# Kernel tuning notes

Hardware: AMD Instinct MI355X
Metric: run time of the kernel (lower is better)

## Reference

```python
import jax, jax.numpy as jnp
import numpy as np

EPS = 1e-5

def _conv(x, w):
    # x: [B,C,H,W], w: [K,C,3,3] -> [B,K,H,W]; stacks all centroid convs into one conv
    return jax.lax.conv_general_dilated(
        x, w, window_strides=(1, 1), padding=((1, 1), (1, 1)),
        dimension_numbers=("NCHW", "OIHW", "NCHW"))

def _bn(x, gamma, beta, mean, var):
    # inference-mode BatchNorm2d over channel axis 1
    inv = gamma / jnp.sqrt(var + EPS)
    return x * inv[None, :, None, None] + (beta - mean * inv)[None, :, None, None]

def setup_inputs() -> dict:
    key = jax.random.key(0)
    ks = jax.random.split(key, 16)
    B, C, H, W, K = 32, 256, 56, 56, 16
    d = {}
    d["x"] = jax.random.normal(ks[0], (B, C, H, W), jnp.float32)
    d["w1"] = jax.random.normal(ks[1], (K, C, 3, 3), jnp.float32) * 0.05
    d["b1"] = jax.random.normal(ks[2], (K,), jnp.float32) * 0.05
    d["w2"] = jax.random.normal(ks[3], (K, C, 3, 3), jnp.float32) * 0.05
    d["b2"] = jax.random.normal(ks[4], (K,), jnp.float32) * 0.05
    d["gamma1"] = jax.random.uniform(ks[5], (C,), jnp.float32)
    d["beta1"] = jax.random.normal(ks[6], (C,), jnp.float32) * 0.1
    d["mean1"] = jax.random.normal(ks[7], (C,), jnp.float32) * 0.1
    d["var1"] = jax.random.uniform(ks[8], (C,), jnp.float32)
    d["gamma2"] = jax.random.uniform(ks[9], (C,), jnp.float32)
    d["beta2"] = jax.random.normal(ks[10], (C,), jnp.float32) * 0.1
    d["mean2"] = jax.random.normal(ks[11], (C,), jnp.float32) * 0.1
    d["var2"] = jax.random.uniform(ks[12], (C,), jnp.float32)
    d["labels1"] = jax.random.randint(ks[13], (C,), 0, K, jnp.int64)
    d["labels2"] = jax.random.randint(ks[14], (C,), 0, K, jnp.int64)
    return d

def reference(x, w1, b1, w2, b2, gamma1, beta1, mean1, var1,
              gamma2, beta2, mean2, var2, labels1, labels2):
    # centroids_apply: run all K centroid convs at once, then label-indexed
    # channel gather (equivalent to the original per-centroid conv + concat)
    y1 = _conv(x, w1)[:, labels1] + b1[labels1][None, :, None, None]
    h = jax.nn.relu(_bn(y1, gamma1, beta1, mean1, var1))
    y2 = _conv(h, w2)[:, labels2] + b2[labels2][None, :, None, None]
    out = _bn(y2, gamma2, beta2, mean2, var2) + x  # identity residual (no skipper)
    return jax.nn.relu(out)
```

## Files before the change

kernel.cpp:

```cpp
#include <hip/hip_runtime.h>
#include <cstddef>
#include <cstdint>

typedef short short8 __attribute__((ext_vector_type(8)));
typedef float f32x4 __attribute__((ext_vector_type(4)));

namespace {
constexpr int B = 32, C = 256, H = 56, W = 56, K = 16;
constexpr int HW = H * W;
constexpr int WP = 58, PP = 58 * 58;
constexpr float EPS = 1e-5f;

constexpr size_t OFF_WF1 = 0;
constexpr size_t OFF_WF2 = 73728;
constexpr size_t OFF_A1 = 147456, OFF_D1 = 148480;
constexpr size_t OFF_A2 = 149504, OFF_D2 = 150528;
constexpr size_t OFF_G1 = 151552, OFF_G2 = 152576;
constexpr size_t OFF_XT = 153600;
constexpr size_t XT_BYTES = (size_t)B * PP * C * 2;
constexpr size_t OFF_HB = OFF_XT + XT_BYTES;
constexpr int BORDER_U4 = 2 * 32 * 228 * 32;
}

__device__ inline ushort f2bf(float f) {
  uint32_t u = __float_as_uint(f);
  u += 0x7fff + ((u >> 16) & 1);
  return (ushort)(u >> 16);
}

__global__ __launch_bounds__(256) void prep_kernel(
    const float* __restrict__ w1, const float* __restrict__ b1,
    const float* __restrict__ w2, const float* __restrict__ b2,
    const float* __restrict__ gamma1, const float* __restrict__ beta1,
    const float* __restrict__ mean1, const float* __restrict__ var1,
    const float* __restrict__ gamma2, const float* __restrict__ beta2,
    const float* __restrict__ mean2, const float* __restrict__ var2,
    const int* __restrict__ lab1, const int* __restrict__ lab2,
    char* __restrict__ wsb) {
  int bid = blockIdx.x, tid = threadIdx.x;
  if (bid < 288) {
    int i = bid * 256 + tid;
    int which = i >= 36864;
    int ii = which ? i - 36864 : i;
    int j = ii & 7, lane = (ii >> 3) & 63, cc = (ii >> 9) & 7, t = ii >> 12;
    int c = cc * 32 + ((lane >> 4) << 3) + j;
    int k = lane & 15;
    const float* w = which ? w2 : w1;
    ushort* wf = (ushort*)(wsb + (which ? OFF_WF2 : OFF_WF1));
    wf[ii] = f2bf(w[k * (C * 9) + c * 9 + t]);
    if (i < C) {
      int g1 = lab1[i], g2 = lab2[i];
      float a1 = gamma1[i] / sqrtf(var1[i] + EPS);
      float a2 = gamma2[i] / sqrtf(var2[i] + EPS);
      ((float*)(wsb + OFF_A1))[i] = a1;
      ((float*)(wsb + OFF_D1))[i] = a1 * b1[g1] + beta1[i] - mean1[i] * a1;
      ((float*)(wsb + OFF_A2))[i] = a2;
      ((float*)(wsb + OFF_D2))[i] = a2 * b2[g2] + beta2[i] - mean2[i] * a2;
      ((int*)(wsb + OFF_G1))[i] = g1;
      ((int*)(wsb + OFF_G2))[i] = g2;
    }
  } else {
    int idx = (bid - 288) * 256 + tid;
    if (idx < BORDER_U4) {
      int which = idx >= (BORDER_U4 / 2);
      int j = which ? idx - BORDER_U4 / 2 : idx;
      int pix = j >> 5, q = j & 31;
      int b = pix / 228, e = pix - b * 228;
      int y, x;
      if (e < 58) { y = 0; x = e; }
      else if (e < 116) { y = 57; x = e - 58; }
      else if (e < 172) { y = e - 115; x = 0; }
      else { y = e - 171; x = 57; }
      size_t off = ((size_t)b * PP + y * WP + x) * C * 2 + (size_t)q * 16;
      int4 z = {0, 0, 0, 0};
      *(int4*)(wsb + (which ? OFF_HB : OFF_XT) + off) = z;
    }
  }
}

__global__ __launch_bounds__(256) void transpose_kernel(
    const float* __restrict__ x, char* __restrict__ wsb) {
  __shared__ float t[64][65];
  int bid = blockIdx.x;
  int b = bid / 196, rem = bid - b * 196, pt = rem >> 2, ct = rem & 3;
  int p0 = pt * 64, c0 = ct * 64;
  int tid = threadIdx.x, lane = tid & 63, grp = tid >> 6;
  const float* xb = x + ((size_t)b * C + c0) * HW + p0;
#pragma unroll
  for (int r = 0; r < 16; ++r) {
    int row = r * 4 + grp;
    t[row][lane] = xb[(size_t)row * HW + lane];
  }
  __syncthreads();
  ushort* xt = (ushort*)(wsb + OFF_XT) + (size_t)b * PP * C;
  int c2 = (tid & 31) * 2, g = tid >> 5;
#pragma unroll
  for (int r = 0; r < 8; ++r) {
    int prow = r * 8 + g;
    int p = p0 + prow;
    int y = p / 56, xx = p - y * 56;
    uint v = (uint)f2bf(t[c2][prow]) | ((uint)f2bf(t[c2 + 1][prow]) << 16);
    *(uint*)(xt + ((size_t)(y + 1) * WP + xx + 1) * C + c0 + c2) = v;
  }
}

__global__ __launch_bounds__(256) void conv1_kernel(char* __restrict__ wsb) {
  __shared__ float zs[128 * 17];
  int tid = threadIdx.x, lane = tid & 63, wave = tid >> 6;
  int row = lane & 15, blk = lane >> 4;
  int gpb = blockIdx.x * 128 + wave * 32;
  const ushort* xt = (const ushort*)(wsb + OFF_XT);
  const ushort* wfl = (const ushort*)(wsb + OFF_WF1) + lane * 8;

  int gp0 = gpb + row, gp1 = gpb + 16 + row;
  int b0 = gp0 / HW, r0 = gp0 - b0 * HW, y0 = r0 / 56, x0 = r0 - y0 * 56;
  int b1_ = gp1 / HW, r1 = gp1 - b1_ * HW, y1 = r1 / 56, x1 = r1 - y1 * 56;
  const ushort* ap0 = xt + ((size_t)b0 * PP + (y0 + 1) * WP + (x0 + 1)) * C;
  const ushort* ap1 = xt + ((size_t)b1_ * PP + (y1 + 1) * WP + (x1 + 1)) * C;

  f32x4 acc0 = {0.f, 0.f, 0.f, 0.f}, acc1 = {0.f, 0.f, 0.f, 0.f};
#pragma unroll
  for (int t = 0; t < 9; ++t) {
    const int toff = ((t / 3 - 1) * WP + (t % 3 - 1)) * C;
#pragma unroll
    for (int cc = 0; cc < 8; ++cc) {
      short8 bf = *(const short8*)(wfl + (t * 8 + cc) * 512);
      int ko = toff + cc * 32 + blk * 8;
      short8 a0 = *(const short8*)(ap0 + ko);
      short8 a1 = *(const short8*)(ap1 + ko);
      acc0 = __builtin_amdgcn_mfma_f32_16x16x32_bf16(a0, bf, acc0, 0, 0, 0);
      acc1 = __builtin_amdgcn_mfma_f32_16x16x32_bf16(a1, bf, acc1, 0, 0, 0);
    }
  }
#pragma unroll
  for (int i = 0; i < 4; ++i) {
    zs[(wave * 32 + blk * 4 + i) * 17 + row] = acc0[i];
    zs[(wave * 32 + 16 + blk * 4 + i) * 17 + row] = acc1[i];
  }
  __syncthreads();

  f32x4 a_ = *(const f32x4*)((const float*)(wsb + OFF_A1) + lane * 4);
  f32x4 d_ = *(const f32x4*)((const float*)(wsb + OFF_D1) + lane * 4);
  int4 g_ = *(const int4*)((const int*)(wsb + OFF_G1) + lane * 4);
  ushort* hb = (ushort*)(wsb + OFF_HB);
  for (int px = 0; px < 32; ++px) {
    int gp = gpb + px;
    int b = gp / HW, r = gp - b * HW, y = r / 56, xx = r - y * 56;
    const float* zr = zs + (wave * 32 + px) * 17;
    float h0 = fmaxf(fmaf(a_.x, zr[g_.x], d_.x), 0.f);
    float h1 = fmaxf(fmaf(a_.y, zr[g_.y], d_.y), 0.f);
    float h2 = fmaxf(fmaf(a_.z, zr[g_.z], d_.z), 0.f);
    float h3 = fmaxf(fmaf(a_.w, zr[g_.w], d_.w), 0.f);
    uint2 v;
    v.x = (uint)f2bf(h0) | ((uint)f2bf(h1) << 16);
    v.y = (uint)f2bf(h2) | ((uint)f2bf(h3) << 16);
    *(uint2*)(hb + ((size_t)b * PP + (y + 1) * WP + (xx + 1)) * C + lane * 4) = v;
  }
}

__global__ __launch_bounds__(256) void conv2_kernel(
    const float* __restrict__ x, char* __restrict__ wsb,
    float* __restrict__ out) {
  __shared__ float zs[128 * 17];
  int tid = threadIdx.x, lane = tid & 63, wave = tid >> 6;
  int row = lane & 15, blk = lane >> 4;
  int gpb = blockIdx.x * 128 + wave * 32;
  const ushort* hbuf = (const ushort*)(wsb + OFF_HB);
  const ushort* wfl = (const ushort*)(wsb + OFF_WF2) + lane * 8;

  int gp0 = gpb + row, gp1 = gpb + 16 + row;
  int b0 = gp0 / HW, r0 = gp0 - b0 * HW, y0 = r0 / 56, x0 = r0 - y0 * 56;
  int b1_ = gp1 / HW, r1 = gp1 - b1_ * HW, y1 = r1 / 56, x1 = r1 - y1 * 56;
  const ushort* ap0 = hbuf + ((size_t)b0 * PP + (y0 + 1) * WP + (x0 + 1)) * C;
  const ushort* ap1 = hbuf + ((size_t)b1_ * PP + (y1 + 1) * WP + (x1 + 1)) * C;

  f32x4 acc0 = {0.f, 0.f, 0.f, 0.f}, acc1 = {0.f, 0.f, 0.f, 0.f};
#pragma unroll
  for (int t = 0; t < 9; ++t) {
    const int toff = ((t / 3 - 1) * WP + (t % 3 - 1)) * C;
#pragma unroll
    for (int cc = 0; cc < 8; ++cc) {
      short8 bf = *(const short8*)(wfl + (t * 8 + cc) * 512);
      int ko = toff + cc * 32 + blk * 8;
      short8 a0 = *(const short8*)(ap0 + ko);
      short8 a1 = *(const short8*)(ap1 + ko);
      acc0 = __builtin_amdgcn_mfma_f32_16x16x32_bf16(a0, bf, acc0, 0, 0, 0);
      acc1 = __builtin_amdgcn_mfma_f32_16x16x32_bf16(a1, bf, acc1, 0, 0, 0);
    }
  }
#pragma unroll
  for (int i = 0; i < 4; ++i) {
    zs[(wave * 32 + blk * 4 + i) * 17 + row] = acc0[i];
    zs[(wave * 32 + 16 + blk * 4 + i) * 17 + row] = acc1[i];
  }
  __syncthreads();

  const float* A2p = (const float*)(wsb + OFF_A2);
  const float* D2p = (const float*)(wsb + OFF_D2);
  const int* G2p = (const int*)(wsb + OFF_G2);
  int pl = lane & 31, ch = lane >> 5;
  int gp = gpb + pl;
  int b = gp / HW, r = gp - b * HW;
  const float* zrow = zs + (wave * 32 + pl) * 17;
  const float* xp = x + (size_t)b * C * HW + r;
  float* op = out + (size_t)b * C * HW + r;
#pragma unroll 4
  for (int cl = 0; cl < 128; ++cl) {
    int c = cl * 2 + ch;
    float a = A2p[c], dd = D2p[c];
    int g = G2p[c];
    float v = fmaf(a, zrow[g], dd) + xp[(size_t)c * HW];
    op[(size_t)c * HW] = fmaxf(v, 0.f);
  }
}

extern "C" void kernel_launch(void* const* d_in, const int* in_sizes, int n_in,
                              void* d_out, int out_size, void* d_ws,
                              size_t ws_size, hipStream_t stream) {
  const float* x = (const float*)d_in[0];
  const float* w1 = (const float*)d_in[1];
  const float* b1 = (const float*)d_in[2];
  const float* w2 = (const float*)d_in[3];
  const float* b2 = (const float*)d_in[4];
  const float* gamma1 = (const float*)d_in[5];
  const float* beta1 = (const float*)d_in[6];
  const float* mean1 = (const float*)d_in[7];
  const float* var1 = (const float*)d_in[8];
  const float* gamma2 = (const float*)d_in[9];
  const float* beta2 = (const float*)d_in[10];
  const float* mean2 = (const float*)d_in[11];
  const float* var2 = (const float*)d_in[12];
  const int* lab1 = (const int*)d_in[13];
  const int* lab2 = (const int*)d_in[14];
  char* wsb = (char*)d_ws;
  float* out = (float*)d_out;

  prep_kernel<<<288 + 1824, 256, 0, stream>>>(
      w1, b1, w2, b2, gamma1, beta1, mean1, var1, gamma2, beta2, mean2, var2,
      lab1, lab2, wsb);
  transpose_kernel<<<32 * 196, 256, 0, stream>>>(x, wsb);
  conv1_kernel<<<(B * HW) / 128, 256, 0, stream>>>(wsb);
  conv2_kernel<<<(B * HW) / 128, 256, 0, stream>>>(x, wsb, out);
}
```

Before: 404.6 us.

## Stage conv inputs in swizzled LDS and store compact 16-channel conv1 outputs

Each conv block now covers two image rows of one batch image. It stages the padded input tile in double-buffered, XOR-swizzled shared memory, so the 3x3 taps reuse LDS data instead of issuing repeated global loads. Conv1 now writes only the raw 16 centroid outputs. Conv2 rebuilds the 256-channel BN+ReLU activation in shared memory from those 16 values, which removes the full bf16 intermediate buffer and its border zeroing. The residual epilogue moves into a separate vectorized kernel. The costs are an extra launch, heavy LDS use that limits occupancy, and idle MFMA slots on one wave because 112 pixels split unevenly across 4 waves.

```diff
diff --git a/kernel.cpp b/kernel.cpp
--- a/kernel.cpp
+++ b/kernel.cpp
@@ -18,8 +18,9 @@
 constexpr size_t OFF_G1 = 151552, OFF_G2 = 152576;
 constexpr size_t OFF_XT = 153600;
 constexpr size_t XT_BYTES = (size_t)B * PP * C * 2;
-constexpr size_t OFF_HB = OFF_XT + XT_BYTES;
-constexpr int BORDER_U4 = 2 * 32 * 228 * 32;
+constexpr size_t OFF_Z1 = OFF_XT + XT_BYTES;
+constexpr size_t OFF_Z2 = OFF_Z1 + (size_t)B * HW * 16 * 4;
+constexpr int BORDER_U4 = 32 * 228 * 32;
 }
 
 __device__ inline ushort f2bf(float f) {
@@ -62,18 +63,16 @@
   } else {
     int idx = (bid - 288) * 256 + tid;
     if (idx < BORDER_U4) {
-      int which = idx >= (BORDER_U4 / 2);
-      int j = which ? idx - BORDER_U4 / 2 : idx;
-      int pix = j >> 5, q = j & 31;
+      int pix = idx >> 5, q = idx & 31;
       int b = pix / 228, e = pix - b * 228;
       int y, x;
       if (e < 58) { y = 0; x = e; }
       else if (e < 116) { y = 57; x = e - 58; }
       else if (e < 172) { y = e - 115; x = 0; }
       else { y = e - 171; x = 57; }
-      size_t off = ((size_t)b * PP + y * WP + x) * C * 2 + (size_t)q * 16;
+      size_t off = OFF_XT + ((size_t)b * PP + y * WP + x) * 512 + (size_t)q * 16;
       int4 z = {0, 0, 0, 0};
-      *(int4*)(wsb + (which ? OFF_HB : OFF_XT) + off) = z;
+      *(int4*)(wsb + off) = z;
     }
   }
 }
@@ -104,113 +103,246 @@
   }
 }
 
-__global__ __launch_bounds__(256) void conv1_kernel(char* __restrict__ wsb) {
-  __shared__ float zs[128 * 17];
-  int tid = threadIdx.x, lane = tid & 63, wave = tid >> 6;
-  int row = lane & 15, blk = lane >> 4;
-  int gpb = blockIdx.x * 128 + wave * 32;
-  const ushort* xt = (const ushort*)(wsb + OFF_XT);
-  const ushort* wfl = (const ushort*)(wsb + OFF_WF1) + lane * 8;
-
-  int gp0 = gpb + row, gp1 = gpb + 16 + row;
-  int b0 = gp0 / HW, r0 = gp0 - b0 * HW, y0 = r0 / 56, x0 = r0 - y0 * 56;
-  int b1_ = gp1 / HW, r1 = gp1 - b1_ * HW, y1 = r1 / 56, x1 = r1 - y1 * 56;
-  const ushort* ap0 = xt + ((size_t)b0 * PP + (y0 + 1) * WP + (x0 + 1)) * C;
-  const ushort* ap1 = xt + ((size_t)b1_ * PP + (y1 + 1) * WP + (x1 + 1)) * C;
-
+__global__ __launch_bounds__(256, 2) void conv1_kernel(char* __restrict__ wsb) {
+  __shared__ char sbuf[59392];
+  const int tid = threadIdx.x, lane = tid & 63, wave = tid >> 6;
+  const int row = lane & 15, blk = lane >> 4;
+  int bid = blockIdx.x;
+  int wg = (bid & 7) * 112 + (bid >> 3);
+  int b = wg / 28, j = wg - b * 28;
+  int y0 = 2 * j;
+  const char* xtb = wsb + OFF_XT + (size_t)b * (PP * C * 2);
+  const char* wf = wsb + OFF_WF1;
+
+  int addrA[2][9][2];
+#pragma unroll
+  for (int f = 0; f < 2; ++f) {
+    int fr = (f == 1) ? (wave + 4) : wave;
+    if (fr > 6) fr = wave;
+    int op = fr * 16 + row;
+    int oy = (op >= 56) ? 1 : 0;
+    int pib = (oy + 1) * 58 + (op - oy * 56) + 1;
+#pragma unroll
+    for (int t = 0; t < 9; ++t) {
+      int pi = pib + (t / 3 - 1) * 58 + (t % 3 - 1);
+      int swz = (pi & 7) << 4;
+      addrA[f][t][0] = pi * 128 + ((blk * 16) ^ swz);
+      addrA[f][t][1] = pi * 128 + ((64 + blk * 16) ^ swz);
+    }
+  }
   f32x4 acc0 = {0.f, 0.f, 0.f, 0.f}, acc1 = {0.f, 0.f, 0.f, 0.f};
-#pragma unroll
-  for (int t = 0; t < 9; ++t) {
-    const int toff = ((t / 3 - 1) * WP + (t % 3 - 1)) * C;
-#pragma unroll
-    for (int cc = 0; cc < 8; ++cc) {
-      short8 bf = *(const short8*)(wfl + (t * 8 + cc) * 512);
-      int ko = toff + cc * 32 + blk * 8;
-      short8 a0 = *(const short8*)(ap0 + ko);
-      short8 a1 = *(const short8*)(ap1 + ko);
-      acc0 = __builtin_amdgcn_mfma_f32_16x16x32_bf16(a0, bf, acc0, 0, 0, 0);
-      acc1 = __builtin_amdgcn_mfma_f32_16x16x32_bf16(a1, bf, acc1, 0, 0, 0);
-    }
-  }
+
+  auto fill = [&](int cc, char* buf) {
+#pragma unroll
+    for (int i = 0; i < 8; ++i) {
+      int idx = i * 256 + tid;
+      if (idx < 1856) {
+        int pi = idx >> 3, sub = idx & 7;
+        int r = pi / 58, xx = pi - r * 58;
+        const char* src =
+            xtb + (((size_t)(y0 + r) * 58 + xx) * 256 + cc * 64) * 2 + sub * 16;
+        int4 v = *(const int4*)src;
+        *(int4*)(buf + pi * 128 + ((sub * 16) ^ ((pi & 7) << 4))) = v;
+      }
+    }
+  };
+  auto mstep = [&](int cc, const char* buf) {
+#pragma unroll
+    for (int t = 0; t < 9; ++t) {
+#pragma unroll
+      for (int ks = 0; ks < 2; ++ks) {
+        short8 bf =
+            *(const short8*)(wf + ((t * 8 + cc * 2 + ks) * 64 + lane) * 16);
+        short8 a0 = *(const short8*)(buf + addrA[0][t][ks]);
+        acc0 = __builtin_amdgcn_mfma_f32_16x16x32_bf16(a0, bf, acc0, 0, 0, 0);
+        if (wave < 3) {
+          short8 a1 = *(const short8*)(buf + addrA[1][t][ks]);
+          acc1 = __builtin_amdgcn_mfma_f32_16x16x32_bf16(a1, bf, acc1, 0, 0, 0);
+        }
+      }
+    }
+  };
+
+  fill(0, sbuf);
+  __syncthreads();
+  for (int cc = 0; cc < 4; ++cc) {
+    if (cc < 3) fill(cc + 1, sbuf + ((cc + 1) & 1) * 29696);
+    mstep(cc, sbuf + (cc & 1) * 29696);
+    __syncthreads();
+  }
+  float* zs = (float*)sbuf;
 #pragma unroll
   for (int i = 0; i < 4; ++i) {
-    zs[(wave * 32 + blk * 4 + i) * 17 + row] = acc0[i];
-    zs[(wave * 32 + 16 + blk * 4 + i) * 17 + row] = acc1[i];
-  }
-  __syncthreads();
-
-  f32x4 a_ = *(const f32x4*)((const float*)(wsb + OFF_A1) + lane * 4);
-  f32x4 d_ = *(const f32x4*)((const float*)(wsb + OFF_D1) + lane * 4);
-  int4 g_ = *(const int4*)((const int*)(wsb + OFF_G1) + lane * 4);
-  ushort* hb = (ushort*)(wsb + OFF_HB);
-  for (int px = 0; px < 32; ++px) {
-    int gp = gpb + px;
-    int b = gp / HW, r = gp - b * HW, y = r / 56, xx = r - y * 56;
-    const float* zr = zs + (wave * 32 + px) * 17;
-    float h0 = fmaxf(fmaf(a_.x, zr[g_.x], d_.x), 0.f);
-    float h1 = fmaxf(fmaf(a_.y, zr[g_.y], d_.y), 0.f);
-    float h2 = fmaxf(fmaf(a_.z, zr[g_.z], d_.z), 0.f);
-    float h3 = fmaxf(fmaf(a_.w, zr[g_.w], d_.w), 0.f);
-    uint2 v;
-    v.x = (uint)f2bf(h0) | ((uint)f2bf(h1) << 16);
-    v.y = (uint)f2bf(h2) | ((uint)f2bf(h3) << 16);
-    *(uint2*)(hb + ((size_t)b * PP + (y + 1) * WP + (xx + 1)) * C + lane * 4) = v;
-  }
-}
-
-__global__ __launch_bounds__(256) void conv2_kernel(
-    const float* __restrict__ x, char* __restrict__ wsb,
+    zs[(wave * 16 + blk * 4 + i) * 17 + row] = acc0[i];
+    if (wave < 3) zs[((wave + 4) * 16 + blk * 4 + i) * 17 + row] = acc1[i];
+  }
+  __syncthreads();
+  float* z1 = (float*)(wsb + OFF_Z1) + ((size_t)b * HW + y0 * 56) * 16;
+#pragma unroll
+  for (int i = 0; i < 2; ++i) {
+    int id = i * 256 + tid;
+    if (id < 448) {
+      int px = id >> 2, q = id & 3;
+      f32x4 v;
+      v.x = zs[px * 17 + q * 4 + 0];
+      v.y = zs[px * 17 + q * 4 + 1];
+      v.z = zs[px * 17 + q * 4 + 2];
+      v.w = zs[px * 17 + q * 4 + 3];
+      *(f32x4*)(z1 + (size_t)id * 4) = v;
+    }
+  }
+}
+
+__global__ __launch_bounds__(256, 2) void conv2_kernel(char* __restrict__ wsb) {
+  __shared__ char sbuf[75168];
+  const int tid = threadIdx.x, lane = tid & 63, wave = tid >> 6;
+  const int row = lane & 15, blk = lane >> 4;
+  int bid = blockIdx.x;
+  int wg = (bid & 7) * 112 + (bid >> 3);
+  int b = wg / 28, j = wg - b * 28;
+  int y0 = 2 * j;
+  const char* wf = wsb + OFF_WF2;
+  float* zt = (float*)(sbuf + 59392);
+
+#pragma unroll
+  for (int i = 0; i < 16; ++i) {
+    int id = i * 256 + tid;
+    if (id < 3944) zt[id] = 0.f;
+  }
+  __syncthreads();
+  const float* z1 = (const float*)(wsb + OFF_Z1) + (size_t)b * HW * 16;
+#pragma unroll
+  for (int i = 0; i < 4; ++i) {
+    int id = i * 256 + tid;
+    if (id < 896) {
+      int r = id / 224, rem = id - r * 224, xx = rem >> 2, q = rem & 3;
+      int yg = y0 - 1 + r;
+      if (yg >= 0 && yg < 56) {
+        f32x4 v = *(const f32x4*)(z1 + ((size_t)yg * 56 + xx) * 16 + q * 4);
+        int base = (r * 58 + xx + 1) * 17 + q * 4;
+        zt[base + 0] = v.x;
+        zt[base + 1] = v.y;
+        zt[base + 2] = v.z;
+        zt[base + 3] = v.w;
+      }
+    }
+  }
+
+  int addrA[2][9][2];
+#pragma unroll
+  for (int f = 0; f < 2; ++f) {
+    int fr = (f == 1) ? (wave + 4) : wave;
+    if (fr > 6) fr = wave;
+    int op = fr * 16 + row;
+    int oy = (op >= 56) ? 1 : 0;
+    int pib = (oy + 1) * 58 + (op - oy * 56) + 1;
+#pragma unroll
+    for (int t = 0; t < 9; ++t) {
+      int pi = pib + (t / 3 - 1) * 58 + (t % 3 - 1);
+      int swz = (pi & 7) << 4;
+      addrA[f][t][0] = pi * 128 + ((blk * 16) ^ swz);
+      addrA[f][t][1] = pi * 128 + ((64 + blk * 16) ^ swz);
+    }
+  }
+  f32x4 acc0 = {0.f, 0.f, 0.f, 0.f}, acc1 = {0.f, 0.f, 0.f, 0.f};
+  const int cp = tid & 31, pig = tid >> 5;
+  const float* A1 = (const float*)(wsb + OFF_A1);
+  const float* D1 = (const float*)(wsb + OFF_D1);
+  const int* G1 = (const int*)(wsb + OFF_G1);
+
+  auto expand = [&](int cc, char* buf) {
+    int c = cc * 64 + cp * 2;
+    float2 a = *(const float2*)(A1 + c);
+    float2 dd = *(const float2*)(D1 + c);
+    int2 g = *(const int2*)(G1 + c);
+#pragma unroll 4
+    for (int i = 0; i < 29; ++i) {
+      int pi = pig + i * 8;
+      float za = zt[pi * 17 + g.x], zb = zt[pi * 17 + g.y];
+      float h0 = fmaxf(fmaf(a.x, za, dd.x), 0.f);
+      float h1 = fmaxf(fmaf(a.y, zb, dd.y), 0.f);
+      uint u = (uint)f2bf(h0) | ((uint)f2bf(h1) << 16);
+      *(uint*)(buf + pi * 128 + ((cp * 4) ^ ((pi & 7) << 4))) = u;
+    }
+  };
+  auto mstep = [&](int cc, const char* buf) {
+#pragma unroll
+    for (int t = 0; t < 9; ++t) {
+#pragma unroll
+      for (int ks = 0; ks < 2; ++ks) {
+        short8 bf =
+            *(const short8*)(wf + ((t * 8 + cc * 2 + ks) * 64 + lane) * 16);
+        short8 a0 = *(const short8*)(buf + addrA[0][t][ks]);
+        acc0 = __builtin_amdgcn_mfma_f32_16x16x32_bf16(a0, bf, acc0, 0, 0, 0);
+        if (wave < 3) {
+          short8 a1 = *(const short8*)(buf + addrA[1][t][ks]);
+          acc1 = __builtin_amdgcn_mfma_f32_16x16x32_bf16(a1, bf, acc1, 0, 0, 0);
+        }
+      }
+    }
+  };
+
+  __syncthreads();
+  expand(0, sbuf);
+  __syncthreads();
+  for (int cc = 0; cc < 4; ++cc) {
+    if (cc < 3) expand(cc + 1, sbuf + ((cc + 1) & 1) * 29696);
+    mstep(cc, sbuf + (cc & 1) * 29696);
+    __syncthreads();
+  }
+  float* zs = (float*)sbuf;
+#pragma unroll
+  for (int i = 0; i < 4; ++i) {
+    zs[(wave * 16 + blk * 4 + i) * 17 + row] = acc0[i];
+    if (wave < 3) zs[((wave + 4) * 16 + blk * 4 + i) * 17 + row] = acc1[i];
+  }
+  __syncthreads();
+  float* z2 = (float*)(wsb + OFF_Z2) + ((size_t)b * HW + y0 * 56) * 16;
+#pragma unroll
+  for (int i = 0; i < 2; ++i) {
+    int id = i * 256 + tid;
+    if (id < 448) {
+      int px = id >> 2, q = id & 3;
+      f32x4 v;
+      v.x = zs[px * 17 + q * 4 + 0];
+      v.y = zs[px * 17 + q * 4 + 1];
+      v.z = zs[px * 17 + q * 4 + 2];
+      v.w = zs[px * 17 + q * 4 + 3];
+      *(f32x4*)(z2 + (size_t)id * 4) = v;
+    }
+  }
+}
+
+__global__ __launch_bounds__(256) void epilogue_kernel(
+    const float* __restrict__ x, const char* __restrict__ wsb,
     float* __restrict__ out) {
-  __shared__ float zs[128 * 17];
-  int tid = threadIdx.x, lane = tid & 63, wave = tid >> 6;
-  int row = lane & 15, blk = lane >> 4;
-  int gpb = blockIdx.x * 128 + wave * 32;
-  const ushort* hbuf = (const ushort*)(wsb + OFF_HB);
-  const ushort* wfl = (const ushort*)(wsb + OFF_WF2) + lane * 8;
-
-  int gp0 = gpb + row, gp1 = gpb + 16 + row;
-  int b0 = gp0 / HW, r0 = gp0 - b0 * HW, y0 = r0 / 56, x0 = r0 - y0 * 56;
-  int b1_ = gp1 / HW, r1 = gp1 - b1_ * HW, y1 = r1 / 56, x1 = r1 - y1 * 56;
-  const ushort* ap0 = hbuf + ((size_t)b0 * PP + (y0 + 1) * WP + (x0 + 1)) * C;
-  const ushort* ap1 = hbuf + ((size_t)b1_ * PP + (y1 + 1) * WP + (x1 + 1)) * C;
-
-  f32x4 acc0 = {0.f, 0.f, 0.f, 0.f}, acc1 = {0.f, 0.f, 0.f, 0.f};
-#pragma unroll
-  for (int t = 0; t < 9; ++t) {
-    const int toff = ((t / 3 - 1) * WP + (t % 3 - 1)) * C;
-#pragma unroll
-    for (int cc = 0; cc < 8; ++cc) {
-      short8 bf = *(const short8*)(wfl + (t * 8 + cc) * 512);
-      int ko = toff + cc * 32 + blk * 8;
-      short8 a0 = *(const short8*)(ap0 + ko);
-      short8 a1 = *(const short8*)(ap1 + ko);
-      acc0 = __builtin_amdgcn_mfma_f32_16x16x32_bf16(a0, bf, acc0, 0, 0, 0);
-      acc1 = __builtin_amdgcn_mfma_f32_16x16x32_bf16(a1, bf, acc1, 0, 0, 0);
-    }
-  }
-#pragma unroll
-  for (int i = 0; i < 4; ++i) {
-    zs[(wave * 32 + blk * 4 + i) * 17 + row] = acc0[i];
-    zs[(wave * 32 + 16 + blk * 4 + i) * 17 + row] = acc1[i];
-  }
-  __syncthreads();
-
-  const float* A2p = (const float*)(wsb + OFF_A2);
-  const float* D2p = (const float*)(wsb + OFF_D2);
-  const int* G2p = (const int*)(wsb + OFF_G2);
-  int pl = lane & 31, ch = lane >> 5;
-  int gp = gpb + pl;
-  int b = gp / HW, r = gp - b * HW;
-  const float* zrow = zs + (wave * 32 + pl) * 17;
-  const float* xp = x + (size_t)b * C * HW + r;
-  float* op = out + (size_t)b * C * HW + r;
+  int bid = blockIdx.x;
+  int wg = (bid & 7) * 112 + (bid >> 3);
+  int b = wg / 28, j = wg - b * 28;
+  int p0 = 2 * j * 56;
+  int tid = threadIdx.x;
+  int q = tid & 31, cg = tid >> 5;
+  bool act = q < 28;
+  const float* A2 = (const float*)(wsb + OFF_A2);
+  const float* D2 = (const float*)(wsb + OFF_D2);
+  const int* G2 = (const int*)(wsb + OFF_G2);
+  const float* z2 = (const float*)(wsb + OFF_Z2) + ((size_t)b * HW + p0) * 16;
+  size_t xb = (size_t)b * C * HW + p0 + q * 4;
 #pragma unroll 4
-  for (int cl = 0; cl < 128; ++cl) {
-    int c = cl * 2 + ch;
-    float a = A2p[c], dd = D2p[c];
-    int g = G2p[c];
-    float v = fmaf(a, zrow[g], dd) + xp[(size_t)c * HW];
-    op[(size_t)c * HW] = fmaxf(v, 0.f);
+  for (int i = 0; i < 32; ++i) {
+    int c = i * 8 + cg;
+    if (act) {
+      float a = A2[c], d = D2[c];
+      int g = G2[c];
+      const float* zr = z2 + q * 64 + g;
+      f32x4 xv = *(const f32x4*)(x + xb + (size_t)c * HW);
+      f32x4 v;
+      v.x = fmaxf(fmaf(a, zr[0], d) + xv.x, 0.f);
+      v.y = fmaxf(fmaf(a, zr[16], d) + xv.y, 0.f);
+      v.z = fmaxf(fmaf(a, zr[32], d) + xv.z, 0.f);
+      v.w = fmaxf(fmaf(a, zr[48], d) + xv.w, 0.f);
+      *(f32x4*)(out + xb + (size_t)c * HW) = v;
+    }
   }
 }
 
@@ -235,10 +367,11 @@
   char* wsb = (char*)d_ws;
   float* out = (float*)d_out;
 
-  prep_kernel<<<288 + 1824, 256, 0, stream>>>(
+  prep_kernel<<<288 + 912, 256, 0, stream>>>(
       w1, b1, w2, b2, gamma1, beta1, mean1, var1, gamma2, beta2, mean2, var2,
       lab1, lab2, wsb);
   transpose_kernel<<<32 * 196, 256, 0, stream>>>(x, wsb);
-  conv1_kernel<<<(B * HW) / 128, 256, 0, stream>>>(wsb);
-  conv2_kernel<<<(B * HW) / 128, 256, 0, stream>>>(x, wsb, out);
-}
+  conv1_kernel<<<896, 256, 0, stream>>>(wsb);
+  conv2_kernel<<<896, 256, 0, stream>>>(wsb);
+  epilogue_kernel<<<896, 256, 0, stream>>>(x, wsb, out);
+}
```

New measurement: 363.5 us. 10.2% less time.
